# Kernel tuning notes

Measured on AMD Instinct MI355X. Metric: run time of the kernel, lower is better.

Reference implementation:

```python
import jax, jax.numpy as jnp
import numpy as np

LOG2 = np.float32(np.log(2.0))

def _jsd_pos(p):
    # get_positive_expectation, measure='JSD', average=False
    return LOG2 - jax.nn.softplus(-p)

def setup_inputs() -> dict:
    key = jax.random.key(0)
    k1, k2, k3, k4, k5, k6 = jax.random.split(key, 6)
    N, G, D = 65536, 512, 256
    batch_1 = jnp.sort(jax.random.randint(k1, (N,), 0, G))
    batch_2 = jnp.sort(jax.random.randint(k2, (N,), 0, G))
    z1 = jax.random.normal(k3, (N, D), dtype=jnp.float32)
    z2 = jax.random.normal(k4, (N, D), dtype=jnp.float32)
    g1 = jax.random.normal(k5, (G, D), dtype=jnp.float32)
    g2 = jax.random.normal(k6, (G, D), dtype=jnp.float32)
    return {"batch_1": batch_1, "batch_2": batch_2, "z1": z1, "z2": z2, "g1": g1, "g2": g2}

def reference(batch_1, batch_2, z1, z2, g1, g2):
    # pos_mask scatter-build -> dense one-hot [N, G]
    pos_mask_1 = jax.nn.one_hot(batch_1, g1.shape[0], dtype=z1.dtype)
    pos_mask_2 = jax.nn.one_hot(batch_2, g2.shape[0], dtype=z2.dtype)
    # masked node-graph similarity matrices [N, G]
    self_sim_1 = (z1 @ g1.T) * pos_mask_1
    self_sim_2 = (z2 @ g2.T) * pos_mask_2
    cross_sim_12 = (z1 @ g2.T) * pos_mask_1
    cross_sim_21 = (z2 @ g1.T) * pos_mask_2
    # sep=True branch: per-node row sums, L2 distance over nodes
    self_js_11 = _jsd_pos(self_sim_1).sum(1)
    cross_js_12 = _jsd_pos(cross_sim_12).sum(1)
    self_js_22 = _jsd_pos(self_sim_2).sum(1)
    cross_js_21 = _jsd_pos(cross_sim_21).sum(1)
    L_1 = jnp.sqrt(jnp.sum((self_js_11 - cross_js_12) ** 2))
    L_2 = jnp.sqrt(jnp.sum((self_js_22 - cross_js_21) ** 2))
    return L_1 + L_2
```

## Files before the change

### kernel.cpp

```cpp
#include <hip/hip_runtime.h>
#include <math.h>

__device__ __forceinline__ float spn(float p) {
    return fmaxf(-p, 0.0f) + __logf(1.0f + __expf(-fabsf(p)));
}

__device__ __forceinline__ float dot4(float4 a, float4 b) {
    return a.x * b.x + a.y * b.y + a.z * b.z + a.w * b.w;
}

__device__ __forceinline__ float wave64_reduce(float x) {
    int t;
    t = __builtin_amdgcn_update_dpp(0, __builtin_bit_cast(int, x), 0x111, 0xf, 0xf, true);
    x += __builtin_bit_cast(float, t);
    t = __builtin_amdgcn_update_dpp(0, __builtin_bit_cast(int, x), 0x112, 0xf, 0xf, true);
    x += __builtin_bit_cast(float, t);
    t = __builtin_amdgcn_update_dpp(0, __builtin_bit_cast(int, x), 0x114, 0xf, 0xf, true);
    x += __builtin_bit_cast(float, t);
    t = __builtin_amdgcn_update_dpp(0, __builtin_bit_cast(int, x), 0x118, 0xf, 0xf, true);
    x += __builtin_bit_cast(float, t);
    t = __builtin_amdgcn_update_dpp(0, __builtin_bit_cast(int, x), 0x142, 0xa, 0xf, true);
    x += __builtin_bit_cast(float, t);
    t = __builtin_amdgcn_update_dpp(0, __builtin_bit_cast(int, x), 0x143, 0xc, 0xf, true);
    x += __builtin_bit_cast(float, t);
    return x;
}

#define NBLOCKS 4096
#define NODES_PER_WAVE 4

__global__ __launch_bounds__(256) void jsd_dot_kernel(
    const int*   __restrict__ b1,
    const int*   __restrict__ b2,
    const float* __restrict__ z1,
    const float* __restrict__ z2,
    const float* __restrict__ g1,
    const float* __restrict__ g2,
    float*       __restrict__ partials)
{
    const int wave = threadIdx.x >> 6;
    const int lane = threadIdx.x & 63;
    const int w    = blockIdx.x * 4 + wave;
    const int base = w * NODES_PER_WAVE;

    const int sbase = __builtin_amdgcn_readfirstlane(base);

    int i1[NODES_PER_WAVE], i2[NODES_PER_WAVE];
    #pragma unroll
    for (int j = 0; j < NODES_PER_WAVE; ++j) {
        i1[j] = b1[sbase + j];
        i2[j] = b2[sbase + j];
    }

    float4 a1[NODES_PER_WAVE], a2[NODES_PER_WAVE];
    #pragma unroll
    for (int j = 0; j < NODES_PER_WAVE; ++j) {
        a1[j] = ((const float4*)(z1 + (size_t)(sbase + j) * 256))[lane];
        a2[j] = ((const float4*)(z2 + (size_t)(sbase + j) * 256))[lane];
    }

    float acc1 = 0.0f, acc2 = 0.0f;

    #pragma unroll
    for (int j = 0; j < NODES_PER_WAVE; ++j) {
        const float4 w11 = ((const float4*)(g1 + (size_t)i1[j] * 256))[lane];
        const float4 w12 = ((const float4*)(g2 + (size_t)i1[j] * 256))[lane];
        const float4 w22 = ((const float4*)(g2 + (size_t)i2[j] * 256))[lane];
        const float4 w21 = ((const float4*)(g1 + (size_t)i2[j] * 256))[lane];

        float s11 = wave64_reduce(dot4(a1[j], w11));
        float c12 = wave64_reduce(dot4(a1[j], w12));
        float s22 = wave64_reduce(dot4(a2[j], w22));
        float c21 = wave64_reduce(dot4(a2[j], w21));

        if (lane == 63) {
            float d1 = spn(c12) - spn(s11);
            float d2 = spn(c21) - spn(s22);
            acc1 += d1 * d1;
            acc2 += d2 * d2;
        }
    }

    __shared__ float s1[4], s2[4];
    if (lane == 63) { s1[wave] = acc1; s2[wave] = acc2; }
    __syncthreads();

    if (threadIdx.x == 0) {
        partials[blockIdx.x * 2 + 0] = s1[0] + s1[1] + s1[2] + s1[3];
        partials[blockIdx.x * 2 + 1] = s2[0] + s2[1] + s2[2] + s2[3];
    }
}

__global__ __launch_bounds__(256) void jsd_reduce_kernel(
    const float* __restrict__ partials,
    float*       __restrict__ out)
{
    const int tid  = threadIdx.x;
    const int wave = tid >> 6;
    const int lane = tid & 63;

    float a = 0.0f, b = 0.0f;
    #pragma unroll
    for (int i = 0; i < NBLOCKS / 256; ++i) {
        a += partials[(i * 256 + tid) * 2 + 0];
        b += partials[(i * 256 + tid) * 2 + 1];
    }

    a = wave64_reduce(a);
    b = wave64_reduce(b);

    __shared__ float s1[4], s2[4];
    if (lane == 63) { s1[wave] = a; s2[wave] = b; }
    __syncthreads();

    if (tid == 0) {
        float t1 = s1[0] + s1[1] + s1[2] + s1[3];
        float t2 = s2[0] + s2[1] + s2[2] + s2[3];
        out[0] = sqrtf(t1) + sqrtf(t2);
    }
}

extern "C" void kernel_launch(void* const* d_in, const int* in_sizes, int n_in,
                              void* d_out, int out_size, void* d_ws, size_t ws_size,
                              hipStream_t stream) {
    const int*   b1 = (const int*)  d_in[0];
    const int*   b2 = (const int*)  d_in[1];
    const float* z1 = (const float*)d_in[2];
    const float* z2 = (const float*)d_in[3];
    const float* g1 = (const float*)d_in[4];
    const float* g2 = (const float*)d_in[5];
    float* out      = (float*)d_out;
    float* partials = (float*)d_ws;

    jsd_dot_kernel<<<NBLOCKS, 256, 0, stream>>>(b1, b2, z1, z2, g1, g2, partials);
    jsd_reduce_kernel<<<1, 256, 0, stream>>>(partials, out);
}
```

Baseline: 154.6 us.

## Compute one node dot product per lane instead of per-wave reductions

Work is remapped so each lane handles one whole node and computes a full 256-long dot product serially, with each of the four waves handling one of the four (z,g) pairings. This removes the four cross-lane DPP reductions per node, and the reduction is done once per block on the squared differences. The cost is that z and g rows are now read with a strided, uncoalesced pattern (each lane walks its own 1 KB row), which may hurt memory efficiency. Each z row is also now loaded by two waves instead of one, relying on cache hits.

Result: slower. 167.3 us (+8.2%).

```diff
diff --git a/kernel.cpp b/kernel.cpp
--- a/kernel.cpp
+++ b/kernel.cpp
@@ -3,10 +3,6 @@
 
 __device__ __forceinline__ float spn(float p) {
     return fmaxf(-p, 0.0f) + __logf(1.0f + __expf(-fabsf(p)));
-}
-
-__device__ __forceinline__ float dot4(float4 a, float4 b) {
-    return a.x * b.x + a.y * b.y + a.z * b.z + a.w * b.w;
 }
 
 __device__ __forceinline__ float wave64_reduce(float x) {
@@ -26,8 +22,7 @@
     return x;
 }
 
-#define NBLOCKS 4096
-#define NODES_PER_WAVE 4
+#define NBLOCKS 1024
 
 __global__ __launch_bounds__(256) void jsd_dot_kernel(
     const int*   __restrict__ b1,
@@ -40,54 +35,46 @@
 {
     const int wave = threadIdx.x >> 6;
     const int lane = threadIdx.x & 63;
-    const int w    = blockIdx.x * 4 + wave;
-    const int base = w * NODES_PER_WAVE;
+    const int node = blockIdx.x * 64 + lane;
 
-    const int sbase = __builtin_amdgcn_readfirstlane(base);
+    const float* zp = (wave < 2) ? z1 : z2;
+    const int*   bp = (wave < 2) ? b1 : b2;
+    const float* gp = (wave == 0 || wave == 3) ? g1 : g2;
 
-    int i1[NODES_PER_WAVE], i2[NODES_PER_WAVE];
-    #pragma unroll
-    for (int j = 0; j < NODES_PER_WAVE; ++j) {
-        i1[j] = b1[sbase + j];
-        i2[j] = b2[sbase + j];
+    const int gi = bp[node];
+
+    const float4* zr = (const float4*)(zp + (size_t)node * 256);
+    const float4* gr = (const float4*)(gp + (size_t)gi   * 256);
+
+    float ax = 0.0f, ay = 0.0f, az = 0.0f, aw = 0.0f;
+    #pragma unroll 8
+    for (int k = 0; k < 64; ++k) {
+        const float4 a = zr[k];
+        const float4 b = gr[k];
+        ax += a.x * b.x;
+        ay += a.y * b.y;
+        az += a.z * b.z;
+        aw += a.w * b.w;
     }
+    const float dot = (ax + ay) + (az + aw);
 
-    float4 a1[NODES_PER_WAVE], a2[NODES_PER_WAVE];
-    #pragma unroll
-    for (int j = 0; j < NODES_PER_WAVE; ++j) {
-        a1[j] = ((const float4*)(z1 + (size_t)(sbase + j) * 256))[lane];
-        a2[j] = ((const float4*)(z2 + (size_t)(sbase + j) * 256))[lane];
-    }
-
-    float acc1 = 0.0f, acc2 = 0.0f;
-
-    #pragma unroll
-    for (int j = 0; j < NODES_PER_WAVE; ++j) {
-        const float4 w11 = ((const float4*)(g1 + (size_t)i1[j] * 256))[lane];
-        const float4 w12 = ((const float4*)(g2 + (size_t)i1[j] * 256))[lane];
-        const float4 w22 = ((const float4*)(g2 + (size_t)i2[j] * 256))[lane];
-        const float4 w21 = ((const float4*)(g1 + (size_t)i2[j] * 256))[lane];
-
-        float s11 = wave64_reduce(dot4(a1[j], w11));
-        float c12 = wave64_reduce(dot4(a1[j], w12));
-        float s22 = wave64_reduce(dot4(a2[j], w22));
-        float c21 = wave64_reduce(dot4(a2[j], w21));
-
-        if (lane == 63) {
-            float d1 = spn(c12) - spn(s11);
-            float d2 = spn(c21) - spn(s22);
-            acc1 += d1 * d1;
-            acc2 += d2 * d2;
-        }
-    }
-
-    __shared__ float s1[4], s2[4];
-    if (lane == 63) { s1[wave] = acc1; s2[wave] = acc2; }
+    __shared__ float part[4][64];
+    part[wave][lane] = dot;
     __syncthreads();
 
-    if (threadIdx.x == 0) {
-        partials[blockIdx.x * 2 + 0] = s1[0] + s1[1] + s1[2] + s1[3];
-        partials[blockIdx.x * 2 + 1] = s2[0] + s2[1] + s2[2] + s2[3];
+    if (wave == 0) {
+        const float s11 = part[0][lane];
+        const float c12 = part[1][lane];
+        const float s22 = part[2][lane];
+        const float c21 = part[3][lane];
+        const float d1 = spn(c12) - spn(s11);
+        const float d2 = spn(c21) - spn(s22);
+        const float e1 = wave64_reduce(d1 * d1);
+        const float e2 = wave64_reduce(d2 * d2);
+        if (lane == 63) {
+            partials[blockIdx.x * 2 + 0] = e1;
+            partials[blockIdx.x * 2 + 1] = e2;
+        }
     }
 }
 
```

## Compute per-node dot products with bf16 MFMA and take the diagonal

Applied to the files above, without the earlier changes.

Replaces the per-node wave-wide fp32 dot products and DPP reductions with 16x16x32 bf16 MFMA tiles. Each wave covers 16 nodes and multiplies them against their gathered graph rows, keeping only the diagonal entries of the result. Operands are rounded from fp32 to bf16 in registers, which lowers precision and spends 15/16 of the MFMA work on off-diagonal products. The memory traffic is unchanged and the kernel is likely bandwidth-bound, so the gain would come from fewer reductions and instructions.

Result: slower. 160.7 us (+4.0%).

```diff
diff --git a/kernel.cpp b/kernel.cpp
--- a/kernel.cpp
+++ b/kernel.cpp
@@ -1,12 +1,25 @@
 #include <hip/hip_runtime.h>
 #include <math.h>
+
+typedef __attribute__((ext_vector_type(8))) short bf16x8;
+typedef __attribute__((ext_vector_type(4))) float f32x4;
 
 __device__ __forceinline__ float spn(float p) {
     return fmaxf(-p, 0.0f) + __logf(1.0f + __expf(-fabsf(p)));
 }
 
-__device__ __forceinline__ float dot4(float4 a, float4 b) {
-    return a.x * b.x + a.y * b.y + a.z * b.z + a.w * b.w;
+__device__ __forceinline__ short bfr(float f) {
+    unsigned u = __builtin_bit_cast(unsigned, f);
+    return (short)((u + 0x8000u) >> 16);
+}
+
+__device__ __forceinline__ bf16x8 cvt8(const float* p) {
+    const float4 lo = ((const float4*)p)[0];
+    const float4 hi = ((const float4*)p)[1];
+    bf16x8 r;
+    r[0] = bfr(lo.x); r[1] = bfr(lo.y); r[2] = bfr(lo.z); r[3] = bfr(lo.w);
+    r[4] = bfr(hi.x); r[5] = bfr(hi.y); r[6] = bfr(hi.z); r[7] = bfr(hi.w);
+    return r;
 }
 
 __device__ __forceinline__ float wave64_reduce(float x) {
@@ -26,10 +39,9 @@
     return x;
 }
 
-#define NBLOCKS 4096
-#define NODES_PER_WAVE 4
+#define NBLK 1024
 
-__global__ __launch_bounds__(256) void jsd_dot_kernel(
+__global__ __launch_bounds__(256) void jsd_mfma_kernel(
     const int*   __restrict__ b1,
     const int*   __restrict__ b2,
     const float* __restrict__ z1,
@@ -40,49 +52,62 @@
 {
     const int wave = threadIdx.x >> 6;
     const int lane = threadIdx.x & 63;
-    const int w    = blockIdx.x * 4 + wave;
-    const int base = w * NODES_PER_WAVE;
+    const int col  = lane & 15;
+    const int quad = lane >> 4;
 
-    const int sbase = __builtin_amdgcn_readfirstlane(base);
+    const int window = blockIdx.x * 4 + wave;
+    const int node   = window * 16 + col;
 
-    int i1[NODES_PER_WAVE], i2[NODES_PER_WAVE];
+    const int i1 = b1[node];
+    const int i2 = b2[node];
+
+    const float* z1r = z1 + (size_t)node * 256 + quad * 8;
+    const float* z2r = z2 + (size_t)node * 256 + quad * 8;
+    const float* p11 = g1 + (size_t)i1 * 256 + quad * 8;
+    const float* p12 = g2 + (size_t)i1 * 256 + quad * 8;
+    const float* p22 = g2 + (size_t)i2 * 256 + quad * 8;
+    const float* p21 = g1 + (size_t)i2 * 256 + quad * 8;
+
+    f32x4 a11 = {0.f, 0.f, 0.f, 0.f};
+    f32x4 a12 = {0.f, 0.f, 0.f, 0.f};
+    f32x4 a22 = {0.f, 0.f, 0.f, 0.f};
+    f32x4 a21 = {0.f, 0.f, 0.f, 0.f};
+
     #pragma unroll
-    for (int j = 0; j < NODES_PER_WAVE; ++j) {
-        i1[j] = b1[sbase + j];
-        i2[j] = b2[sbase + j];
+    for (int c = 0; c < 8; ++c) {
+        const int o = c * 32;
+        const bf16x8 va1 = cvt8(z1r + o);
+        const bf16x8 va2 = cvt8(z2r + o);
+        const bf16x8 w11 = cvt8(p11 + o);
+        const bf16x8 w12 = cvt8(p12 + o);
+        const bf16x8 w22 = cvt8(p22 + o);
+        const bf16x8 w21 = cvt8(p21 + o);
+        a11 = __builtin_amdgcn_mfma_f32_16x16x32_bf16(va1, w11, a11, 0, 0, 0);
+        a12 = __builtin_amdgcn_mfma_f32_16x16x32_bf16(va1, w12, a12, 0, 0, 0);
+        a22 = __builtin_amdgcn_mfma_f32_16x16x32_bf16(va2, w22, a22, 0, 0, 0);
+        a21 = __builtin_amdgcn_mfma_f32_16x16x32_bf16(va2, w21, a21, 0, 0, 0);
     }
 
-    float4 a1[NODES_PER_WAVE], a2[NODES_PER_WAVE];
-    #pragma unroll
-    for (int j = 0; j < NODES_PER_WAVE; ++j) {
-        a1[j] = ((const float4*)(z1 + (size_t)(sbase + j) * 256))[lane];
-        a2[j] = ((const float4*)(z2 + (size_t)(sbase + j) * 256))[lane];
-    }
+    const bool owner = (quad == (col >> 2));
+    const int  reg   = col & 3;
+    auto sel = [&](f32x4 v) -> float {
+        float x = v[0];
+        x = (reg == 1) ? v[1] : x;
+        x = (reg == 2) ? v[2] : x;
+        x = (reg == 3) ? v[3] : x;
+        return x;
+    };
 
-    float acc1 = 0.0f, acc2 = 0.0f;
+    const float d1 = spn(sel(a12)) - spn(sel(a11));
+    const float d2 = spn(sel(a21)) - spn(sel(a22));
+    float e1 = owner ? d1 * d1 : 0.0f;
+    float e2 = owner ? d2 * d2 : 0.0f;
 
-    #pragma unroll
-    for (int j = 0; j < NODES_PER_WAVE; ++j) {
-        const float4 w11 = ((const float4*)(g1 + (size_t)i1[j] * 256))[lane];
-        const float4 w12 = ((const float4*)(g2 + (size_t)i1[j] * 256))[lane];
-        const float4 w22 = ((const float4*)(g2 + (size_t)i2[j] * 256))[lane];
-        const float4 w21 = ((const float4*)(g1 + (size_t)i2[j] * 256))[lane];
-
-        float s11 = wave64_reduce(dot4(a1[j], w11));
-        float c12 = wave64_reduce(dot4(a1[j], w12));
-        float s22 = wave64_reduce(dot4(a2[j], w22));
-        float c21 = wave64_reduce(dot4(a2[j], w21));
-
-        if (lane == 63) {
-            float d1 = spn(c12) - spn(s11);
-            float d2 = spn(c21) - spn(s22);
-            acc1 += d1 * d1;
-            acc2 += d2 * d2;
-        }
-    }
+    e1 = wave64_reduce(e1);
+    e2 = wave64_reduce(e2);
 
     __shared__ float s1[4], s2[4];
-    if (lane == 63) { s1[wave] = acc1; s2[wave] = acc2; }
+    if (lane == 63) { s1[wave] = e1; s2[wave] = e2; }
     __syncthreads();
 
     if (threadIdx.x == 0) {
@@ -101,7 +126,7 @@
 
     float a = 0.0f, b = 0.0f;
     #pragma unroll
-    for (int i = 0; i < NBLOCKS / 256; ++i) {
+    for (int i = 0; i < NBLK / 256; ++i) {
         a += partials[(i * 256 + tid) * 2 + 0];
         b += partials[(i * 256 + tid) * 2 + 1];
     }
@@ -132,6 +157,6 @@
     float* out      = (float*)d_out;
     float* partials = (float*)d_ws;
 
-    jsd_dot_kernel<<<NBLOCKS, 256, 0, stream>>>(b1, b2, z1, z2, g1, g2, partials);
+    jsd_mfma_kernel<<<NBLK, 256, 0, stream>>>(b1, b2, z1, z2, g1, g2, partials);
     jsd_reduce_kernel<<<1, 256, 0, stream>>>(partials, out);
 }
```
